# Optimization experiments

Hardware: AMD Instinct MI355X
Metric: run time of the kernel (lower is better)

## Reference

```python
import jax, jax.numpy as jnp
import numpy as np

N_QUBITS = 4
LAYERS = 2
NUM_HEADS = 8
EMBED = 32
DK = EMBED // NUM_HEADS  # == N_QUBITS
B, S = 32, 4096


def _ry(t):
    c, s = jnp.cos(t / 2), jnp.sin(t / 2)
    m = jnp.stack([jnp.stack([c, -s], -1), jnp.stack([s, c], -1)], -2)
    return m.astype(jnp.complex64)


def _rx(t):
    c = jnp.cos(t / 2).astype(jnp.complex64)
    s = (-1j) * jnp.sin(t / 2).astype(jnp.complex64)
    return jnp.stack([jnp.stack([c, s], -1), jnp.stack([s, c], -1)], -2)


def _rz(t):
    em = jnp.exp(-0.5j * t.astype(jnp.complex64))
    ep = jnp.conj(em)
    z = jnp.zeros_like(em)
    return jnp.stack([jnp.stack([em, z], -1), jnp.stack([z, ep], -1)], -2)


def _apply_1q(state, U, w, n):
    # state: (B, 2**n); wire 0 is the most-significant bit (PennyLane convention)
    s = state.reshape(-1, 2 ** w, 2, 2 ** (n - 1 - w))
    if U.ndim == 2:  # shared gate
        s = jnp.einsum('ij,bpjq->bpiq', U, s)
    else:  # per-token gate, U: (B,2,2)
        s = jnp.einsum('bij,bpjq->bpiq', U, s)
    return s.reshape(-1, 2 ** n)


def _cnot(state, c, t, n):
    s = state.reshape((-1,) + (2,) * n)
    c_ax, t_ax = 1 + c, 1 + t
    s0 = jax.lax.slice_in_dim(s, 0, 1, axis=c_ax)
    s1 = jax.lax.slice_in_dim(s, 1, 2, axis=c_ax)
    s1 = jnp.flip(s1, axis=t_ax)  # X on target where control == 1
    s = jnp.concatenate([s0, s1], axis=c_ax)
    return s.reshape(-1, 2 ** n)


def _z_expvals(state, n):
    p = jnp.abs(state) ** 2  # (B, 2**n)
    outs = []
    for i in range(n):
        pr = p.reshape(-1, 2 ** i, 2, 2 ** (n - 1 - i))
        outs.append(pr[:, :, 0, :].sum((1, 2)) - pr[:, :, 1, :].sum((1, 2)))
    return jnp.stack(outs, -1)  # (B, n)


def _head_fwd(x_h, p_h):
    # x_h: (BT, n_qubits) angles, p_h: (layers, n_qubits, 3)
    n, L = N_QUBITS, LAYERS
    bt = x_h.shape[0]
    state = jnp.zeros((bt, 2 ** n), jnp.complex64).at[:, 0].set(1.0)
    for i in range(n):
        state = _apply_1q(state, _ry(x_h[:, i]), i, n)
    for l in range(L):
        for i in range(n):
            state = _apply_1q(state, _rx(p_h[l, i, 0]), i, n)
            state = _apply_1q(state, _ry(p_h[l, i, 1]), i, n)
            state = _apply_1q(state, _rz(p_h[l, i, 2]), i, n)
        for i in range(n - 1):
            state = _cnot(state, i, i + 1, n)
        state = _cnot(state, n - 1, 0, n)
    return _z_expvals(state, n)


def setup_inputs() -> dict:
    key = jax.random.key(0)
    k1, k2, k3, k4 = jax.random.split(key, 4)
    x = jax.random.normal(k1, (B, S, EMBED), jnp.float32)
    params = jax.random.normal(k2, (NUM_HEADS, LAYERS, N_QUBITS, 3), jnp.float32)
    fan_in = NUM_HEADS * N_QUBITS
    bound = 1.0 / np.sqrt(fan_in)
    W_out = jax.random.uniform(k3, (EMBED, fan_in), jnp.float32, -bound, bound)
    b_out = jax.random.uniform(k4, (EMBED,), jnp.float32, -bound, bound)
    return {'x': x, 'params': params, 'W_out': W_out, 'b_out': b_out}


def reference(x, params, W_out, b_out):
    b, s, e = x.shape
    xh = x.reshape(b, s, NUM_HEADS, DK)
    xh = jnp.moveaxis(xh, 2, 0).reshape(NUM_HEADS, b * s, DK)  # (H, BT, d_k)
    ang = xh[:, :, :N_QUBITS]  # angles fed into RY embedding
    ev = jax.vmap(_head_fwd)(ang, params)  # (H, BT, n_qubits)
    concat = jnp.moveaxis(ev, 0, 1).reshape(b, s, NUM_HEADS * N_QUBITS)
    return concat @ W_out.T + b_out
```

## Files before the change

kernel.cpp:

```cpp
#include <hip/hip_runtime.h>
#include <math.h>

#define NQ   4
#define NH   8
#define NL   2
#define DIM  16
#define EMB  32
#define TPB  64
#define EVP  33

using cfloat = const __attribute__((address_space(4))) float;
__device__ __forceinline__ cfloat* cptr(const float* p) {
    return (cfloat*)(unsigned long long)p;
}

__global__ void build_unitaries_kernel(const float* __restrict__ params,
                                       float* __restrict__ Uws) {
    int tid = threadIdx.x;
    int h   = tid >> 4;
    int col = tid & 15;

    float re[DIM], im[DIM];
#pragma unroll
    for (int j = 0; j < DIM; ++j) { re[j] = (j == col) ? 1.f : 0.f; im[j] = 0.f; }

#pragma unroll
    for (int l = 0; l < NL; ++l) {
#pragma unroll
        for (int q = 0; q < NQ; ++q) {
            const float* p = params + ((h * NL + l) * NQ + q) * 3;
            const int m = 1 << (3 - q);
            {
                float s, c; __sincosf(0.5f * p[0], &s, &c);
#pragma unroll
                for (int j = 0; j < DIM; ++j) {
                    if (j & m) continue;
                    const int j1 = j | m;
                    float r0 = re[j], i0 = im[j], r1 = re[j1], i1 = im[j1];
                    re[j]  = c * r0 + s * i1;
                    im[j]  = c * i0 - s * r1;
                    re[j1] = s * i0 + c * r1;
                    im[j1] = -s * r0 + c * i1;
                }
            }
            {
                float s, c; __sincosf(0.5f * p[1], &s, &c);
#pragma unroll
                for (int j = 0; j < DIM; ++j) {
                    if (j & m) continue;
                    const int j1 = j | m;
                    float r0 = re[j], i0 = im[j], r1 = re[j1], i1 = im[j1];
                    re[j]  = c * r0 - s * r1;
                    im[j]  = c * i0 - s * i1;
                    re[j1] = s * r0 + c * r1;
                    im[j1] = s * i0 + c * i1;
                }
            }
            {
                float s, c; __sincosf(0.5f * p[2], &s, &c);
#pragma unroll
                for (int j = 0; j < DIM; ++j) {
                    if (j & m) continue;
                    const int j1 = j | m;
                    float r0 = re[j], i0 = im[j], r1 = re[j1], i1 = im[j1];
                    re[j]  = c * r0 + s * i0;
                    im[j]  = c * i0 - s * r0;
                    re[j1] = c * r1 - s * i1;
                    im[j1] = c * i1 + s * r1;
                }
            }
        }
#pragma unroll
        for (int e = 0; e < NQ; ++e) {
            const int cm = 1 << (3 - e), tm = 1 << (3 - ((e + 1) & 3));
#pragma unroll
            for (int j = 0; j < DIM; ++j) {
                if ((j & cm) && !(j & tm)) {
                    const int j1 = j | tm;
                    float tr = re[j]; re[j] = re[j1]; re[j1] = tr;
                    float ti = im[j]; im[j] = im[j1]; im[j1] = ti;
                }
            }
        }
    }
#pragma unroll
    for (int j = 0; j < DIM; ++j) {
        Uws[(h * DIM + j) * DIM + col]        = re[j];
        Uws[2048 + (h * DIM + j) * DIM + col] = im[j];
    }
}

__global__ __launch_bounds__(512, 4)
void qmha_kernel(const float* __restrict__ x,
                 const float* __restrict__ Uws,
                 const float* __restrict__ W,
                 const float* __restrict__ bvec,
                 float* __restrict__ out) {
    __shared__ float evs[TPB * EVP];

    const int tid  = threadIdx.x;
    const int tok0 = blockIdx.x * TPB;
    const int lane = tid & 63;

    {
        const int h = __builtin_amdgcn_readfirstlane(tid >> 6);
        const int tok = tok0 + lane;

        const float4 xa = *(const float4*)(x + (size_t)tok * EMB + h * NQ);
        float c0, s0, c1, s1, c2, s2, c3, s3;
        __sincosf(0.5f * xa.x, &s0, &c0);
        __sincosf(0.5f * xa.y, &s1, &c1);
        __sincosf(0.5f * xa.z, &s2, &c2);
        __sincosf(0.5f * xa.w, &s3, &c3);

        float p01[4], p23[4], a[DIM];
        p01[0] = c0 * c1; p01[1] = c0 * s1; p01[2] = s0 * c1; p01[3] = s0 * s1;
        p23[0] = c2 * c3; p23[1] = c2 * s3; p23[2] = s2 * c3; p23[3] = s2 * s3;
#pragma unroll
        for (int j = 0; j < DIM; ++j) a[j] = p01[j >> 2] * p23[j & 3];

        cfloat* Ur = cptr(Uws + h * 256);
        cfloat* Ui = cptr(Uws + 2048 + h * 256);

        float ev0 = 0.f, ev1 = 0.f, ev2 = 0.f, ev3 = 0.f;
#pragma unroll
        for (int j = 0; j < DIM; ++j) {
            float ar = 0.f, ai = 0.f;
#pragma unroll
            for (int k = 0; k < DIM; ++k) {
                ar = fmaf(Ur[j * DIM + k], a[k], ar);
                ai = fmaf(Ui[j * DIM + k], a[k], ai);
            }
            const float pj = ar * ar + ai * ai;
            ev0 += (j & 8) ? -pj : pj;
            ev1 += (j & 4) ? -pj : pj;
            ev2 += (j & 2) ? -pj : pj;
            ev3 += (j & 1) ? -pj : pj;
        }

        evs[lane * EVP + h * 4 + 0] = ev0;
        evs[lane * EVP + h * 4 + 1] = ev1;
        evs[lane * EVP + h * 4 + 2] = ev2;
        evs[lane * EVP + h * 4 + 3] = ev3;
    }
    __syncthreads();

    {
        const int w  = __builtin_amdgcn_readfirstlane(tid >> 6);
        const int e0 = w * 4;

        cfloat* Wr = cptr(W);
        cfloat* bc = cptr(bvec);

        float o0 = bc[e0 + 0], o1 = bc[e0 + 1], o2 = bc[e0 + 2], o3 = bc[e0 + 3];
#pragma unroll
        for (int k = 0; k < EMB; ++k) {
            const float evk = evs[lane * EVP + k];
            o0 = fmaf(Wr[(e0 + 0) * EMB + k], evk, o0);
            o1 = fmaf(Wr[(e0 + 1) * EMB + k], evk, o1);
            o2 = fmaf(Wr[(e0 + 2) * EMB + k], evk, o2);
            o3 = fmaf(Wr[(e0 + 3) * EMB + k], evk, o3);
        }
        float4 v; v.x = o0; v.y = o1; v.z = o2; v.w = o3;
        *(float4*)(out + (size_t)(tok0 + lane) * EMB + e0) = v;
    }
}

extern "C" void kernel_launch(void* const* d_in, const int* in_sizes, int n_in,
                              void* d_out, int out_size, void* d_ws, size_t ws_size,
                              hipStream_t stream) {
    const float* x      = (const float*)d_in[0];
    const float* params = (const float*)d_in[1];
    const float* W_out  = (const float*)d_in[2];
    const float* b_out  = (const float*)d_in[3];
    float*       out    = (float*)d_out;
    float*       Uws    = (float*)d_ws;

    const int ntok = in_sizes[0] / EMB;

    hipLaunchKernelGGL(build_unitaries_kernel, dim3(1), dim3(128), 0, stream,
                       params, Uws);

    hipLaunchKernelGGL(qmha_kernel, dim3(ntok / TPB), dim3(512), 0, stream,
                       x, Uws, W_out, b_out, out);
}
```

Baseline: 95.27 us.

## Precompute Pauli-basis expectation tensors so each token needs only a small bilinear form

Adds a per-head precompute kernel that turns the circuit unitary into a Pauli-basis tensor E (4 qubits × 81 coefficients). The expectation values become a product-state contraction over {1, cos x, sin x} features. Per token this replaces the 16x16 complex matrix-vector product and squared magnitudes with about 324 FMAs per head using full-angle sincos. The cost is an extra small kernel launch and more scalar constant loads per token.

```diff
diff --git a/kernel.cpp b/kernel.cpp
--- a/kernel.cpp
+++ b/kernel.cpp
@@ -8,6 +8,7 @@
 #define EMB  32
 #define TPB  64
 #define EVP  33
+#define EHS  328
 
 using cfloat = const __attribute__((address_space(4))) float;
 __device__ __forceinline__ cfloat* cptr(const float* p) {
@@ -90,9 +91,55 @@
     }
 }
 
+__global__ void build_E_kernel(const float* __restrict__ Uws,
+                               float* __restrict__ Ews) {
+    const int h   = blockIdx.x;
+    const int tid = threadIdx.x;
+    __shared__ float Urs[256], Uis[256];
+    if (tid < 256) {
+        Urs[tid] = Uws[h * 256 + tid];
+        Uis[tid] = Uws[2048 + h * 256 + tid];
+    }
+    __syncthreads();
+    if (tid >= 324) return;
+
+    const int q  = tid / 81;
+    const int ab = tid % 81;
+    const int a = ab / 9, b = ab % 9;
+    const int t0 = a / 3, t1 = a % 3, t2 = b / 3, t3 = b % 3;
+
+    float Sv[16];
+#pragma unroll
+    for (int m = 0; m < 16; ++m) Sv[m] = 0.f;
+
+    for (int c = 0; c < 16; ++c) {
+        const int o0 = (c >> 3) & 1, o1 = (c >> 2) & 1;
+        const int o2 = (c >> 1) & 1, o3 = c & 1;
+        float sg = 1.f;
+        const int bk0 = (t0 == 2) ? (1 - o0) : o0; if (t0 == 1 && o0) sg = -sg;
+        const int bk1 = (t1 == 2) ? (1 - o1) : o1; if (t1 == 1 && o1) sg = -sg;
+        const int bk2 = (t2 == 2) ? (1 - o2) : o2; if (t2 == 1 && o2) sg = -sg;
+        const int bk3 = (t3 == 2) ? (1 - o3) : o3; if (t3 == 1 && o3) sg = -sg;
+        const int j = (o0 << 3) | (o1 << 2) | (o2 << 1) | o3;
+        const int k = (bk0 << 3) | (bk1 << 2) | (bk2 << 1) | bk3;
+#pragma unroll
+        for (int m = 0; m < 16; ++m) {
+            const float v = Urs[m * 16 + j] * Urs[m * 16 + k]
+                          + Uis[m * 16 + j] * Uis[m * 16 + k];
+            Sv[m] = fmaf(sg, v, Sv[m]);
+        }
+    }
+    float acc = 0.f;
+#pragma unroll
+    for (int m = 0; m < 16; ++m)
+        acc += ((m >> (3 - q)) & 1) ? -Sv[m] : Sv[m];
+
+    Ews[h * EHS + tid] = acc * 0.0625f;
+}
+
 __global__ __launch_bounds__(512, 4)
 void qmha_kernel(const float* __restrict__ x,
-                 const float* __restrict__ Uws,
+                 const float* __restrict__ Ews,
                  const float* __restrict__ W,
                  const float* __restrict__ bvec,
                  float* __restrict__ out) {
@@ -107,41 +154,35 @@
         const int tok = tok0 + lane;
 
         const float4 xa = *(const float4*)(x + (size_t)tok * EMB + h * NQ);
-        float c0, s0, c1, s1, c2, s2, c3, s3;
-        __sincosf(0.5f * xa.x, &s0, &c0);
-        __sincosf(0.5f * xa.y, &s1, &c1);
-        __sincosf(0.5f * xa.z, &s2, &c2);
-        __sincosf(0.5f * xa.w, &s3, &c3);
-
-        float p01[4], p23[4], a[DIM];
-        p01[0] = c0 * c1; p01[1] = c0 * s1; p01[2] = s0 * c1; p01[3] = s0 * s1;
-        p23[0] = c2 * c3; p23[1] = c2 * s3; p23[2] = s2 * c3; p23[3] = s2 * s3;
-#pragma unroll
-        for (int j = 0; j < DIM; ++j) a[j] = p01[j >> 2] * p23[j & 3];
-
-        cfloat* Ur = cptr(Uws + h * 256);
-        cfloat* Ui = cptr(Uws + 2048 + h * 256);
-
-        float ev0 = 0.f, ev1 = 0.f, ev2 = 0.f, ev3 = 0.f;
-#pragma unroll
-        for (int j = 0; j < DIM; ++j) {
-            float ar = 0.f, ai = 0.f;
-#pragma unroll
-            for (int k = 0; k < DIM; ++k) {
-                ar = fmaf(Ur[j * DIM + k], a[k], ar);
-                ai = fmaf(Ui[j * DIM + k], a[k], ai);
-            }
-            const float pj = ar * ar + ai * ai;
-            ev0 += (j & 8) ? -pj : pj;
-            ev1 += (j & 4) ? -pj : pj;
-            ev2 += (j & 2) ? -pj : pj;
-            ev3 += (j & 1) ? -pj : pj;
-        }
-
-        evs[lane * EVP + h * 4 + 0] = ev0;
-        evs[lane * EVP + h * 4 + 1] = ev1;
-        evs[lane * EVP + h * 4 + 2] = ev2;
-        evs[lane * EVP + h * 4 + 3] = ev3;
+        float C0, S0, C1, S1, C2, S2, C3, S3;
+        __sincosf(xa.x, &S0, &C0);
+        __sincosf(xa.y, &S1, &C1);
+        __sincosf(xa.z, &S2, &C2);
+        __sincosf(xa.w, &S3, &C3);
+
+        float m01[9], m23[9];
+        m01[0] = 1.f; m01[1] = C1;      m01[2] = S1;
+        m01[3] = C0;  m01[4] = C0 * C1; m01[5] = C0 * S1;
+        m01[6] = S0;  m01[7] = S0 * C1; m01[8] = S0 * S1;
+        m23[0] = 1.f; m23[1] = C3;      m23[2] = S3;
+        m23[3] = C2;  m23[4] = C2 * C3; m23[5] = C2 * S3;
+        m23[6] = S2;  m23[7] = S2 * C3; m23[8] = S2 * S3;
+
+        cfloat* E = cptr(Ews + h * EHS);
+
+#pragma unroll
+        for (int q = 0; q < NQ; ++q) {
+            float acc = 0.f;
+#pragma unroll
+            for (int a = 0; a < 9; ++a) {
+                float inner = 0.f;
+#pragma unroll
+                for (int b = 0; b < 9; ++b)
+                    inner = fmaf(E[q * 81 + a * 9 + b], m23[b], inner);
+                acc = fmaf(m01[a], inner, acc);
+            }
+            evs[lane * EVP + h * 4 + q] = acc;
+        }
     }
     __syncthreads();
 
@@ -175,12 +216,14 @@
     const float* b_out  = (const float*)d_in[3];
     float*       out    = (float*)d_out;
     float*       Uws    = (float*)d_ws;
+    float*       Ews    = (float*)d_ws + 4096;
 
     const int ntok = in_sizes[0] / EMB;
 
     hipLaunchKernelGGL(build_unitaries_kernel, dim3(1), dim3(128), 0, stream,
                        params, Uws);
-
+    hipLaunchKernelGGL(build_E_kernel, dim3(NH), dim3(384), 0, stream,
+                       Uws, Ews);
     hipLaunchKernelGGL(qmha_kernel, dim3(ntok / TPB), dim3(512), 0, stream,
-                       x, Uws, W_out, b_out, out);
-}
+                       x, Ews, W_out, b_out, out);
+}
```

After: 100.2 us. 5.1% more time.
